# Kernel tuning notes

Measured on AMD Instinct MI355X. Metric: run time of the kernel, lower is better.

The kernel has to match this reference:

```python
import jax, jax.numpy as jnp
import numpy as np

EMBED_DIM = 1024
N_HEADS = 16
HEAD_DIM = EMBED_DIM // N_HEADS
EPS = 1e-6


def setup_inputs() -> dict:
    key = jax.random.key(0)
    k_x, k_wqkv, k_bqkv, k_wo, k_bo = jax.random.split(key, 5)
    B, T, C = 2, 2048, EMBED_DIM
    s = 1.0 / np.sqrt(C)
    return {
        "x": jax.random.normal(k_x, (B, T, C), dtype=jnp.float32),
        "w_qkv": jax.random.normal(k_wqkv, (C, 3 * C), dtype=jnp.float32) * s,
        "b_qkv": jax.random.normal(k_bqkv, (3 * C,), dtype=jnp.float32) * s,
        "w_out": jax.random.normal(k_wo, (C, C), dtype=jnp.float32) * s,
        "b_out": jax.random.normal(k_bo, (C,), dtype=jnp.float32) * s,
    }


def reference(x, w_qkv, b_qkv, w_out, b_out):
    B, T, C = x.shape
    H, D = N_HEADS, HEAD_DIM
    qkv = x @ w_qkv + b_qkv                       # [B,T,3C]
    q, k, v = jnp.split(qkv, 3, axis=-1)
    # [B,H,T,D]
    q = q.reshape(B, T, H, D).transpose(0, 2, 1, 3)
    k = k.reshape(B, T, H, D).transpose(0, 2, 1, 3)
    v = v.reshape(B, T, H, D).transpose(0, 2, 1, 3)
    dot = jnp.einsum("bhqd,bhkd->bhqk", q, k)     # [B,H,T,T]
    q_sq = jnp.sum(q * q, axis=-1)[..., :, None]  # [B,H,T,1]
    k_sq = jnp.sum(k * k, axis=-1)[..., None, :]  # [B,H,1,T]
    scores = (dot * dot) / (q_sq + k_sq - 2.0 * dot + EPS)
    causal = jnp.tril(jnp.ones((T, T), dtype=bool))
    scores = jnp.where(causal, scores, -jnp.inf)
    attn = jax.nn.softmax(scores, axis=-1)
    out = jnp.einsum("bhqk,bhkd->bhqd", attn, v)  # [B,H,T,D]
    out = out.transpose(0, 2, 1, 3).reshape(B, T, C)
    return out @ w_out + b_out
```

## Files before the change

### kernel.cpp

```cpp
#include <hip/hip_runtime.h>
#include <stdint.h>


#define TSEQ 2048
#define BATCH 2

typedef _Float16 f16x8 __attribute__((ext_vector_type(8)));
typedef _Float16 f16x2h __attribute__((ext_vector_type(2)));
typedef __fp16 fp16x2 __attribute__((ext_vector_type(2)));
typedef float f32x4 __attribute__((ext_vector_type(4)));
typedef unsigned int u32x2 __attribute__((ext_vector_type(2)));

#define MFMA16(a, b, c) __builtin_amdgcn_mfma_f32_16x16x32_f16(a, b, c, 0, 0, 0)

__device__ __forceinline__ unsigned short f2h(float f) {
  union { _Float16 h; unsigned short u; } v;
  v.h = (_Float16)f;
  return v.u;
}
__device__ __forceinline__ unsigned int pack2h(float lo, float hi) {
  return (unsigned int)f2h(lo) | ((unsigned int)f2h(hi) << 16);
}
__device__ __forceinline__ float dot2acc(unsigned int u, float acc) {
  union { unsigned int u; f16x2h h; } c;
  c.u = u;
  return __builtin_amdgcn_fdot2(c.h, c.h, acc, false);
}
__device__ __forceinline__ void async_ld16(const void* g, const void* l) {
  __builtin_amdgcn_global_load_lds((const __attribute__((address_space(1))) void*)g,
                                   (__attribute__((address_space(3))) void*)l,
                                   16, 0, 0);
}
__device__ __forceinline__ unsigned int pk_f16(float lo, float hi) {
  union { fp16x2 h; unsigned int u; } c;
  c.h = __builtin_amdgcn_cvt_pkrtz(lo, hi);
  return c.u;
}

__global__ __launch_bounds__(256) void prep(const float* __restrict__ x,
                                            unsigned short* __restrict__ xh,
                                            const float* __restrict__ w_qkv,
                                            unsigned short* __restrict__ wqkvT,
                                            const float* __restrict__ w_out,
                                            unsigned short* __restrict__ woT) {
  __shared__ unsigned short tile[32][33];
  const int bid = blockIdx.x, tid = threadIdx.x;
  if (bid < 2048) {
    const int i = (bid * 256 + tid) * 8;
    const float4 a = *(const float4*)(x + i);
    const float4 b = *(const float4*)(x + i + 4);
    uint4 o;
    o.x = pack2h(a.x, a.y); o.y = pack2h(a.z, a.w);
    o.z = pack2h(b.x, b.y); o.w = pack2h(b.z, b.w);
    *(uint4*)(xh + i) = o;
    return;
  }
  const bool qkv = bid < 5120;
  const int b2 = qkv ? bid - 2048 : bid - 5120;
  const int NB = qkv ? 96 : 32;
  const int N = NB * 32, K = 1024;
  const float* src = qkv ? w_qkv : w_out;
  unsigned short* dst = qkv ? wqkvT : woT;
  const int nb = (b2 % NB) * 32, kb = (b2 / NB) * 32;
  const int tx = tid & 31, ty = tid >> 5;
#pragma unroll
  for (int i = 0; i < 4; i++)
    tile[ty + 8 * i][tx] = f2h(src[(size_t)(kb + ty + 8 * i) * N + nb + tx]);
  __syncthreads();
#pragma unroll
  for (int i = 0; i < 4; i++)
    dst[(size_t)(nb + ty + 8 * i) * K + kb + tx] = tile[tx][ty + 8 * i];
}

template <int TN, bool OUT_F32>
__global__ __launch_bounds__(256) void gemm_bt(const unsigned short* __restrict__ A,
                                               const unsigned short* __restrict__ Bt,
                                               const float* __restrict__ bias,
                                               void* __restrict__ Cp,
                                               int N, int K) {
  __shared__ __attribute__((aligned(16))) unsigned short Atile[128 * 32];
  __shared__ __attribute__((aligned(16))) unsigned short Btile[TN * 32];
  constexpr int NJ = TN / 32;
  const int tid = threadIdx.x;
  const int w = tid >> 6, lane = tid & 63;
  const int quad = lane >> 4, l15 = lane & 15;
  const int m0 = blockIdx.y * 128, n0 = blockIdx.x * TN;
  const int wr = w >> 1, wc = w & 1;
  const int nwc = wc * (TN / 2);
  f32x4 acc[4][NJ] = {};
  for (int kt = 0; kt < K; kt += 32) {
    __syncthreads();
#pragma unroll
    for (int it = 0; it < 2; it++) {
      const int c = it * 256 + tid;
      async_ld16(A + (size_t)(m0 + (c >> 2)) * K + kt + (c & 3) * 8,
                 &Atile[(size_t)(it * 256 + w * 64) * 8]);
    }
#pragma unroll
    for (int it = 0; it < TN / 64; it++) {
      const int c = it * 256 + tid;
      async_ld16(Bt + (size_t)(n0 + (c >> 2)) * K + kt + (c & 3) * 8,
                 &Btile[(size_t)(it * 256 + w * 64) * 8]);
    }
    __syncthreads();
    f16x8 af[4], bfr[NJ];
#pragma unroll
    for (int i = 0; i < 4; i++)
      af[i] = *(const f16x8*)&Atile[(wr * 64 + i * 16 + l15) * 32 + quad * 8];
#pragma unroll
    for (int j = 0; j < NJ; j++)
      bfr[j] = *(const f16x8*)&Btile[(nwc + j * 16 + l15) * 32 + quad * 8];
#pragma unroll
    for (int i = 0; i < 4; i++)
#pragma unroll
      for (int j = 0; j < NJ; j++)
        acc[i][j] = MFMA16(af[i], bfr[j], acc[i][j]);
  }
#pragma unroll
  for (int j = 0; j < NJ; j++) {
    const int n = n0 + nwc + j * 16 + l15;
    const float bv = bias[n];
#pragma unroll
    for (int i = 0; i < 4; i++) {
      const int mb = m0 + wr * 64 + i * 16 + quad * 4;
#pragma unroll
      for (int r = 0; r < 4; r++) {
        if constexpr (OUT_F32)
          ((float*)Cp)[(size_t)(mb + r) * N + n] = acc[i][j][r] + bv;
        else
          ((unsigned short*)Cp)[(size_t)(mb + r) * N + n] = f2h(acc[i][j][r] + bv);
      }
    }
  }
}

__global__ __launch_bounds__(256, 4) void yat_attn(const unsigned short* __restrict__ qkv,
                                                   unsigned short* __restrict__ outp) {
  __shared__ __attribute__((aligned(16))) unsigned short Kp[2][64 * 72];
  __shared__ __attribute__((aligned(16))) unsigned short Vt[2][64 * 72];
  __shared__ float qsq[64], ksq[2][64];
  const int tid = threadIdx.x;
  const int w = tid >> 6, lane = tid & 63;
  const int quad = lane >> 4, l15 = lane & 15;
  const int bh = blockIdx.x, b = bh >> 4, h = bh & 15;
  const int y = blockIdx.y;
  const int qt = (y < 8) ? 31 - y : (y < 16) ? y - 8 : (y < 24) ? 39 - y : y - 16;
  const unsigned short* base = qkv + (size_t)b * TSEQ * 3072 + h * 64;
  const int t = tid >> 2, dc = (tid & 3) * 16;
  const int d0 = tid & 31, tg8 = tid >> 5;

  uint4 kreg0, kreg1;
  unsigned int vreg[8];
  {
    const unsigned short* gk = base + 1024 + (size_t)t * 3072 + dc;
    kreg0 = *(const uint4*)gk;
    kreg1 = *(const uint4*)(gk + 8);
    const unsigned short* gv = base + 2048 + (size_t)(tg8 * 8) * 3072 + 2 * d0;
#pragma unroll
    for (int s = 0; s < 8; s++)
      vreg[s] = *(const unsigned int*)(gv + (size_t)s * 3072);
  }
  {
    const unsigned short* g = base + (size_t)(qt * 64 + t) * 3072 + dc;
    uint4 v0 = *(const uint4*)g;
    uint4 v1 = *(const uint4*)(g + 8);
    *(uint4*)&Kp[1][t * 72 + dc] = v0;
    *(uint4*)&Kp[1][t * 72 + dc + 8] = v1;
    float s = dot2acc(v0.x, 0.f);
    s = dot2acc(v0.y, s); s = dot2acc(v0.z, s); s = dot2acc(v0.w, s);
    s = dot2acc(v1.x, s); s = dot2acc(v1.y, s); s = dot2acc(v1.z, s);
    s = dot2acc(v1.w, s);
    s += __shfl_xor(s, 1);
    s += __shfl_xor(s, 2);
    if ((tid & 3) == 0) qsq[t] = s;
  }
  auto commit = [&](int buf) {
    *(uint4*)&Kp[buf][t * 72 + dc] = kreg0;
    *(uint4*)&Kp[buf][t * 72 + dc + 8] = kreg1;
    float s = dot2acc(kreg0.x, 0.f);
    s = dot2acc(kreg0.y, s); s = dot2acc(kreg0.z, s); s = dot2acc(kreg0.w, s);
    s = dot2acc(kreg1.x, s); s = dot2acc(kreg1.y, s); s = dot2acc(kreg1.z, s);
    s = dot2acc(kreg1.w, s);
    s += __shfl_xor(s, 1);
    s += __shfl_xor(s, 2);
    if ((tid & 3) == 0) ksq[buf][t] = s;
    uint4 LO, HI;
    LO.x = __builtin_amdgcn_perm(vreg[1], vreg[0], 0x05040100u);
    HI.x = __builtin_amdgcn_perm(vreg[1], vreg[0], 0x07060302u);
    LO.y = __builtin_amdgcn_perm(vreg[3], vreg[2], 0x05040100u);
    HI.y = __builtin_amdgcn_perm(vreg[3], vreg[2], 0x07060302u);
    LO.z = __builtin_amdgcn_perm(vreg[5], vreg[4], 0x05040100u);
    HI.z = __builtin_amdgcn_perm(vreg[5], vreg[4], 0x07060302u);
    LO.w = __builtin_amdgcn_perm(vreg[7], vreg[6], 0x05040100u);
    HI.w = __builtin_amdgcn_perm(vreg[7], vreg[6], 0x07060302u);
    *(uint4*)&Vt[buf][(2 * d0) * 72 + tg8 * 8] = LO;
    *(uint4*)&Vt[buf][(2 * d0 + 1) * 72 + tg8 * 8] = HI;
  };
  commit(0);
  if (qt >= 1) {
    const unsigned short* gk = base + 1024 + (size_t)(64 + t) * 3072 + dc;
    kreg0 = *(const uint4*)gk;
    kreg1 = *(const uint4*)(gk + 8);
    const unsigned short* gv = base + 2048 + (size_t)(64 + tg8 * 8) * 3072 + 2 * d0;
#pragma unroll
    for (int s = 0; s < 8; s++)
      vreg[s] = *(const unsigned int*)(gv + (size_t)s * 3072);
  }
  __syncthreads();
  const f16x8 aq0 = *(const f16x8*)&Kp[1][(w * 16 + l15) * 72 + quad * 8];
  const f16x8 aq1 = *(const f16x8*)&Kp[1][(w * 16 + l15) * 72 + 32 + quad * 8];
  const f16x8 onesf = {(_Float16)1.f, (_Float16)1.f, (_Float16)1.f, (_Float16)1.f,
                       (_Float16)1.f, (_Float16)1.f, (_Float16)1.f, (_Float16)1.f};
  const int ql = w * 16 + l15;
  const float qsq_eps = qsq[ql] + 1e-6f;
  __syncthreads();

  f32x4 accO[4] = {};
  float m_run = 0.f;
  float l_acc = 0.f;

  for (int kt = 0; kt <= qt; kt++) {
    const int cur = kt & 1;
    f32x4 accS[4] = {};
#pragma unroll
    for (int nt = 0; nt < 4; nt++) {
      const f16x8 bk0 = *(const f16x8*)&Kp[cur][(nt * 16 + l15) * 72 + quad * 8];
      const f16x8 bk1 = *(const f16x8*)&Kp[cur][(nt * 16 + l15) * 72 + 32 + quad * 8];
      accS[nt] = MFMA16(bk0, aq0, accS[nt]);
      accS[nt] = MFMA16(bk1, aq1, accS[nt]);
    }
    float pv[4][4];
#pragma unroll
    for (int nt = 0; nt < 4; nt++) {
      const f32x4 k4 = *(const f32x4*)&ksq[cur][nt * 16 + quad * 4];
#pragma unroll
      for (int r = 0; r < 4; r++) {
        const float d = accS[nt][r];
        const float den = __builtin_fmaf(-2.f, d, k4[r] + qsq_eps);
        pv[nt][r] = d * d * __builtin_amdgcn_rcpf(den);
      }
    }
    if (kt == qt) {
#pragma unroll
      for (int nt = 0; nt < 4; nt++)
#pragma unroll
        for (int r = 0; r < 4; r++)
          if (nt * 16 + quad * 4 + r > ql) pv[nt][r] = -1e30f;
    }
    float tm = fmaxf(fmaxf(fmaxf(pv[0][0], pv[0][1]), fmaxf(pv[0][2], pv[0][3])),
                     fmaxf(fmaxf(pv[1][0], pv[1][1]), fmaxf(pv[1][2], pv[1][3])));
    tm = fmaxf(tm, fmaxf(fmaxf(fmaxf(pv[2][0], pv[2][1]), fmaxf(pv[2][2], pv[2][3])),
                         fmaxf(fmaxf(pv[3][0], pv[3][1]), fmaxf(pv[3][2], pv[3][3]))));
    tm = fmaxf(tm, __shfl_xor(tm, 16));
    tm = fmaxf(tm, __shfl_xor(tm, 32));
    const float mn = fmaxf(m_run, tm);
    const float alpha = __expf(m_run - mn);
    m_run = mn;
    unsigned int pa[4], pb[4];
#pragma unroll
    for (int nt = 0; nt < 4; nt++) {
      pa[nt] = pk_f16(__expf(pv[nt][0] - mn), __expf(pv[nt][1] - mn));
      pb[nt] = pk_f16(__expf(pv[nt][2] - mn), __expf(pv[nt][3] - mn));
    }
    if (kt < qt) commit(cur ^ 1);
    if (kt + 2 <= qt) {
      const unsigned short* gk = base + 1024 + (size_t)((kt + 2) * 64 + t) * 3072 + dc;
      kreg0 = *(const uint4*)gk;
      kreg1 = *(const uint4*)(gk + 8);
      const unsigned short* gv =
          base + 2048 + (size_t)((kt + 2) * 64 + tg8 * 8) * 3072 + 2 * d0;
#pragma unroll
      for (int s = 0; s < 8; s++)
        vreg[s] = *(const unsigned int*)(gv + (size_t)s * 3072);
    }
    union { f16x8 v; unsigned int u[4]; } bp0, bp1;
    {
      u32x2 s0 = __builtin_amdgcn_permlane32_swap(pa[0], pa[1], false, false);
      u32x2 s1 = __builtin_amdgcn_permlane16_swap(s0.x, s0.y, false, false);
      bp0.u[0] = s1.x; bp0.u[2] = s1.y;
      s0 = __builtin_amdgcn_permlane32_swap(pb[0], pb[1], false, false);
      s1 = __builtin_amdgcn_permlane16_swap(s0.x, s0.y, false, false);
      bp0.u[1] = s1.x; bp0.u[3] = s1.y;
      s0 = __builtin_amdgcn_permlane32_swap(pa[2], pa[3], false, false);
      s1 = __builtin_amdgcn_permlane16_swap(s0.x, s0.y, false, false);
      bp1.u[0] = s1.x; bp1.u[2] = s1.y;
      s0 = __builtin_amdgcn_permlane32_swap(pb[2], pb[3], false, false);
      s1 = __builtin_amdgcn_permlane16_swap(s0.x, s0.y, false, false);
      bp1.u[1] = s1.x; bp1.u[3] = s1.y;
    }
#pragma unroll
    for (int i = 0; i < 4; i++) {
      accO[i][0] *= alpha; accO[i][1] *= alpha;
      accO[i][2] *= alpha; accO[i][3] *= alpha;
    }
    f32x4 accL = {};
    accL = MFMA16(onesf, bp0.v, accL);
    accL = MFMA16(onesf, bp1.v, accL);
#pragma unroll
    for (int i = 0; i < 4; i++) {
      const f16x8 av0 = *(const f16x8*)&Vt[cur][(i * 16 + l15) * 72 + quad * 8];
      const f16x8 av1 = *(const f16x8*)&Vt[cur][(i * 16 + l15) * 72 + 32 + quad * 8];
      accO[i] = MFMA16(av0, bp0.v, accO[i]);
      accO[i] = MFMA16(av1, bp1.v, accO[i]);
    }
    l_acc = l_acc * alpha + accL[0];
    __syncthreads();
  }

  const float linv = 1.0f / l_acc;
#pragma unroll
  for (int i = 0; i < 4; i++)
#pragma unroll
    for (int r = 0; r < 4; r++)
      Kp[0][(w * 16 + l15) * 72 + i * 16 + quad * 4 + r] = f2h(accO[i][r] * linv);
  __syncthreads();
  {
    uint4 o0 = *(const uint4*)&Kp[0][t * 72 + dc];
    uint4 o1 = *(const uint4*)&Kp[0][t * 72 + dc + 8];
    unsigned short* g = outp + (size_t)(b * TSEQ + qt * 64 + t) * 1024 + h * 64 + dc;
    *(uint4*)g = o0;
    *(uint4*)(g + 8) = o1;
  }
}

extern "C" void kernel_launch(void* const* d_in, const int* in_sizes, int n_in,
                              void* d_out, int out_size, void* d_ws, size_t ws_size,
                              hipStream_t stream) {
  (void)in_sizes; (void)n_in; (void)out_size; (void)ws_size;
  const float* x     = (const float*)d_in[0];
  const float* w_qkv = (const float*)d_in[1];
  const float* b_qkv = (const float*)d_in[2];
  const float* w_out = (const float*)d_in[3];
  const float* b_out = (const float*)d_in[4];
  float* out = (float*)d_out;

  unsigned short* wqkvT  = (unsigned short*)d_ws;
  unsigned short* woT    = wqkvT + (size_t)3072 * 1024;
  unsigned short* qkvws  = woT + (size_t)1024 * 1024;
  unsigned short* xh     = qkvws + (size_t)4096 * 3072;
  unsigned short* attnws = xh;

  prep<<<dim3(6144), 256, 0, stream>>>(x, xh, w_qkv, wqkvT, w_out, woT);
  gemm_bt<128, false><<<dim3(3072 / 128, 4096 / 128), 256, 0, stream>>>(xh, wqkvT, b_qkv, qkvws, 3072, 1024);
  yat_attn<<<dim3(BATCH * 16, 32), 256, 0, stream>>>(qkvws, attnws);
  gemm_bt<64, true><<<dim3(1024 / 64, 4096 / 128), 256, 0, stream>>>(attnws, woT, b_out, out, 1024, 1024);
}
```

Measured before the change: 189.8 us.

## Split long causal query tiles across two blocks and merge partials

Result: slower. 200.5 us (+5.6%).

```diff
diff --git a/kernel.cpp b/kernel.cpp
--- a/kernel.cpp
+++ b/kernel.cpp
@@ -13,10 +13,28 @@
 
 #define MFMA16(a, b, c) __builtin_amdgcn_mfma_f32_16x16x32_f16(a, b, c, 0, 0, 0)
 
+#define WI(q, a, b) ((unsigned)(q) | ((unsigned)(a) << 8) | ((unsigned)(b) << 16))
+__device__ __constant__ unsigned int WMAP[40] = {
+    WI(23, 0, 24), WI(22, 0, 23), WI(21, 0, 22), WI(20, 0, 21),
+    WI(19, 0, 20), WI(18, 0, 19), WI(17, 0, 18), WI(16, 0, 17),
+    WI(28, 14, 29), WI(29, 15, 30), WI(29, 0, 15), WI(30, 0, 15),
+    WI(15, 0, 16), WI(30, 15, 31), WI(31, 16, 32), WI(31, 0, 16),
+    WI(14, 0, 15), WI(28, 0, 14), WI(27, 0, 14), WI(27, 14, 28),
+    WI(26, 13, 27), WI(13, 0, 14), WI(26, 0, 13), WI(25, 0, 13),
+    WI(8, 0, 9), WI(9, 0, 10), WI(10, 0, 11), WI(11, 0, 12),
+    WI(24, 0, 12), WI(12, 0, 13), WI(24, 12, 25), WI(25, 13, 26),
+    WI(0, 0, 1), WI(1, 0, 2), WI(2, 0, 3), WI(3, 0, 4),
+    WI(4, 0, 5), WI(5, 0, 6), WI(6, 0, 7), WI(7, 0, 8)};
+
 __device__ __forceinline__ unsigned short f2h(float f) {
   union { _Float16 h; unsigned short u; } v;
   v.h = (_Float16)f;
   return v.u;
+}
+__device__ __forceinline__ float h2f(unsigned int u) {
+  union { unsigned short u; _Float16 h; } v;
+  v.u = (unsigned short)u;
+  return (float)v.h;
 }
 __device__ __forceinline__ unsigned int pack2h(float lo, float hi) {
   return (unsigned int)f2h(lo) | ((unsigned int)f2h(hi) << 16);
@@ -135,7 +153,8 @@
 }
 
 __global__ __launch_bounds__(256, 4) void yat_attn(const unsigned short* __restrict__ qkv,
-                                                   unsigned short* __restrict__ outp) {
+                                                   unsigned short* __restrict__ outp,
+                                                   unsigned short* __restrict__ part) {
   __shared__ __attribute__((aligned(16))) unsigned short Kp[2][64 * 72];
   __shared__ __attribute__((aligned(16))) unsigned short Vt[2][64 * 72];
   __shared__ float qsq[64], ksq[2][64];
@@ -143,8 +162,8 @@
   const int w = tid >> 6, lane = tid & 63;
   const int quad = lane >> 4, l15 = lane & 15;
   const int bh = blockIdx.x, b = bh >> 4, h = bh & 15;
-  const int y = blockIdx.y;
-  const int qt = (y < 8) ? 31 - y : (y < 16) ? y - 8 : (y < 24) ? 39 - y : y - 16;
+  const unsigned int wi = WMAP[blockIdx.y];
+  const int qt = wi & 255, kb = (wi >> 8) & 255, ke = wi >> 16;
   const unsigned short* base = qkv + (size_t)b * TSEQ * 3072 + h * 64;
   const int t = tid >> 2, dc = (tid & 3) * 16;
   const int d0 = tid & 31, tg8 = tid >> 5;
@@ -152,10 +171,10 @@
   uint4 kreg0, kreg1;
   unsigned int vreg[8];
   {
-    const unsigned short* gk = base + 1024 + (size_t)t * 3072 + dc;
+    const unsigned short* gk = base + 1024 + (size_t)(kb * 64 + t) * 3072 + dc;
     kreg0 = *(const uint4*)gk;
     kreg1 = *(const uint4*)(gk + 8);
-    const unsigned short* gv = base + 2048 + (size_t)(tg8 * 8) * 3072 + 2 * d0;
+    const unsigned short* gv = base + 2048 + (size_t)(kb * 64 + tg8 * 8) * 3072 + 2 * d0;
 #pragma unroll
     for (int s = 0; s < 8; s++)
       vreg[s] = *(const unsigned int*)(gv + (size_t)s * 3072);
@@ -197,11 +216,12 @@
     *(uint4*)&Vt[buf][(2 * d0 + 1) * 72 + tg8 * 8] = HI;
   };
   commit(0);
-  if (qt >= 1) {
-    const unsigned short* gk = base + 1024 + (size_t)(64 + t) * 3072 + dc;
+  if (kb + 1 < ke) {
+    const unsigned short* gk = base + 1024 + (size_t)((kb + 1) * 64 + t) * 3072 + dc;
     kreg0 = *(const uint4*)gk;
     kreg1 = *(const uint4*)(gk + 8);
-    const unsigned short* gv = base + 2048 + (size_t)(64 + tg8 * 8) * 3072 + 2 * d0;
+    const unsigned short* gv =
+        base + 2048 + (size_t)((kb + 1) * 64 + tg8 * 8) * 3072 + 2 * d0;
 #pragma unroll
     for (int s = 0; s < 8; s++)
       vreg[s] = *(const unsigned int*)(gv + (size_t)s * 3072);
@@ -219,8 +239,8 @@
   float m_run = 0.f;
   float l_acc = 0.f;
 
-  for (int kt = 0; kt <= qt; kt++) {
-    const int cur = kt & 1;
+  for (int kt = kb; kt < ke; kt++) {
+    const int cur = (kt - kb) & 1;
     f32x4 accS[4] = {};
 #pragma unroll
     for (int nt = 0; nt < 4; nt++) {
@@ -262,8 +282,8 @@
       pa[nt] = pk_f16(__expf(pv[nt][0] - mn), __expf(pv[nt][1] - mn));
       pb[nt] = pk_f16(__expf(pv[nt][2] - mn), __expf(pv[nt][3] - mn));
     }
-    if (kt < qt) commit(cur ^ 1);
-    if (kt + 2 <= qt) {
+    if (kt + 1 < ke) commit(cur ^ 1);
+    if (kt + 2 < ke) {
       const unsigned short* gk = base + 1024 + (size_t)((kt + 2) * 64 + t) * 3072 + dc;
       kreg0 = *(const uint4*)gk;
       kreg1 = *(const uint4*)(gk + 8);
@@ -307,20 +327,79 @@
     __syncthreads();
   }
 
-  const float linv = 1.0f / l_acc;
-#pragma unroll
-  for (int i = 0; i < 4; i++)
-#pragma unroll
-    for (int r = 0; r < 4; r++)
-      Kp[0][(w * 16 + l15) * 72 + i * 16 + quad * 4 + r] = f2h(accO[i][r] * linv);
-  __syncthreads();
-  {
+  if (kb == 0 && ke == qt + 1) {
+    const float linv = 1.0f / l_acc;
+#pragma unroll
+    for (int i = 0; i < 4; i++)
+#pragma unroll
+      for (int r = 0; r < 4; r++)
+        Kp[0][(w * 16 + l15) * 72 + i * 16 + quad * 4 + r] = f2h(accO[i][r] * linv);
+    __syncthreads();
     uint4 o0 = *(const uint4*)&Kp[0][t * 72 + dc];
     uint4 o1 = *(const uint4*)&Kp[0][t * 72 + dc + 8];
     unsigned short* g = outp + (size_t)(b * TSEQ + qt * 64 + t) * 1024 + h * 64 + dc;
     *(uint4*)g = o0;
     *(uint4*)(g + 8) = o1;
-  }
+  } else {
+    const int sp = qt - 24, hh = kb > 0;
+    unsigned short* ps = part + (size_t)((bh * 8 + sp) * 2 + hh) * 4352;
+    uint4 o0, o1;
+    o0.x = pack2h(accO[0][0], accO[0][1]); o0.y = pack2h(accO[0][2], accO[0][3]);
+    o0.z = pack2h(accO[1][0], accO[1][1]); o0.w = pack2h(accO[1][2], accO[1][3]);
+    o1.x = pack2h(accO[2][0], accO[2][1]); o1.y = pack2h(accO[2][2], accO[2][3]);
+    o1.z = pack2h(accO[3][0], accO[3][1]); o1.w = pack2h(accO[3][2], accO[3][3]);
+    *(uint4*)(ps + (w * 64 + lane) * 16) = o0;
+    *(uint4*)(ps + (w * 64 + lane) * 16 + 8) = o1;
+    if (quad == 0) {
+      ((float*)(ps + 4096))[w * 16 + l15] = l_acc;
+      ((float*)(ps + 4224))[w * 16 + l15] = m_run;
+    }
+  }
+}
+
+__global__ __launch_bounds__(256) void merge_attn(const unsigned short* __restrict__ part,
+                                                  unsigned short* __restrict__ outp) {
+  __shared__ __attribute__((aligned(16))) unsigned short Tr[64 * 72];
+  const int tid = threadIdx.x;
+  const int w = tid >> 6, lane = tid & 63;
+  const int quad = lane >> 4, l15 = lane & 15;
+  const int bh = blockIdx.x, sp = blockIdx.y;
+  const int b = bh >> 4, h = bh & 15;
+  const int qt = 24 + sp;
+  const unsigned short* pa = part + (size_t)((bh * 8 + sp) * 2 + 0) * 4352;
+  const unsigned short* pb = part + (size_t)((bh * 8 + sp) * 2 + 1) * 4352;
+  const uint4 a0 = *(const uint4*)(pa + (w * 64 + lane) * 16);
+  const uint4 a1 = *(const uint4*)(pa + (w * 64 + lane) * 16 + 8);
+  const uint4 b0 = *(const uint4*)(pb + (w * 64 + lane) * 16);
+  const uint4 b1 = *(const uint4*)(pb + (w * 64 + lane) * 16 + 8);
+  const float la = ((const float*)(pa + 4096))[w * 16 + l15];
+  const float ma = ((const float*)(pa + 4224))[w * 16 + l15];
+  const float lb = ((const float*)(pb + 4096))[w * 16 + l15];
+  const float mb = ((const float*)(pb + 4224))[w * 16 + l15];
+  const float m = fmaxf(ma, mb);
+  const float aa = __expf(ma - m), ab = __expf(mb - m);
+  const float linv = 1.0f / (la * aa + lb * ab);
+  const unsigned int ua[8] = {a0.x, a0.y, a0.z, a0.w, a1.x, a1.y, a1.z, a1.w};
+  const unsigned int ub[8] = {b0.x, b0.y, b0.z, b0.w, b1.x, b1.y, b1.z, b1.w};
+#pragma unroll
+  for (int i = 0; i < 4; i++) {
+#pragma unroll
+    for (int r = 0; r < 4; r++) {
+      const unsigned int wa = ua[i * 2 + (r >> 1)];
+      const unsigned int wb = ub[i * 2 + (r >> 1)];
+      const float va = h2f((r & 1) ? (wa >> 16) : (wa & 0xffffu));
+      const float vb = h2f((r & 1) ? (wb >> 16) : (wb & 0xffffu));
+      Tr[(w * 16 + l15) * 72 + i * 16 + quad * 4 + r] =
+          f2h((va * aa + vb * ab) * linv);
+    }
+  }
+  __syncthreads();
+  const int t = tid >> 2, dc = (tid & 3) * 16;
+  uint4 o0 = *(const uint4*)&Tr[t * 72 + dc];
+  uint4 o1 = *(const uint4*)&Tr[t * 72 + dc + 8];
+  unsigned short* g = outp + (size_t)(b * TSEQ + qt * 64 + t) * 1024 + h * 64 + dc;
+  *(uint4*)g = o0;
+  *(uint4*)(g + 8) = o1;
 }
 
 extern "C" void kernel_launch(void* const* d_in, const int* in_sizes, int n_in,
@@ -339,9 +418,11 @@
   unsigned short* qkvws  = woT + (size_t)1024 * 1024;
   unsigned short* xh     = qkvws + (size_t)4096 * 3072;
   unsigned short* attnws = xh;
+  unsigned short* partws = wqkvT;
 
   prep<<<dim3(6144), 256, 0, stream>>>(x, xh, w_qkv, wqkvT, w_out, woT);
   gemm_bt<128, false><<<dim3(3072 / 128, 4096 / 128), 256, 0, stream>>>(xh, wqkvT, b_qkv, qkvws, 3072, 1024);
-  yat_attn<<<dim3(BATCH * 16, 32), 256, 0, stream>>>(qkvws, attnws);
+  yat_attn<<<dim3(BATCH * 16, 40), 256, 0, stream>>>(qkvws, attnws, partws);
+  merge_attn<<<dim3(BATCH * 16, 8), 256, 0, stream>>>(partws, attnws);
   gemm_bt<64, true><<<dim3(1024 / 64, 4096 / 128), 256, 0, stream>>>(attnws, woT, b_out, out, 1024, 1024);
 }
```
